# Kernel tuning notes

Measured on AMD Instinct MI355X. Metric: run time of the kernel, lower is better.

Reference implementation:

```python
import jax, jax.numpy as jnp
import numpy as np

B, S, D_IN, D_OUT, H = 8, 512, 1024, 1024, 8
D_ATT = D_OUT // H
NEG_INF = -1e30


def setup_inputs() -> dict:
    key = jax.random.key(0)
    k1, k2, k3, k4 = jax.random.split(key, 4)
    stdv = 1.0 / np.sqrt(D_OUT)
    return {
        "x": jax.random.normal(k1, (B, S, D_IN), dtype=jnp.float32),
        "mask": jnp.ones((B, S), dtype=jnp.float32),
        "adjacency": jax.random.randint(k2, (B, S, S), 0, 2, dtype=jnp.int32),
        "W": jax.random.uniform(k3, (D_IN, D_OUT), dtype=jnp.float32, minval=-stdv, maxval=stdv),
        "att_w": jax.random.normal(k4, (2 * D_ATT,), dtype=jnp.float32) * 0.05,
        "att_b": jnp.zeros((), dtype=jnp.float32),
    }


def reference(x, mask, adjacency, W, att_w, att_b):
    # projection: [B,S,D_IN] @ [D_IN,D_OUT]
    xp = jnp.einsum("bsi,io->bso", x, W)
    # split heads -> [B,H,S,d]
    xh = xp.reshape(B, S, H, D_ATT).transpose(0, 2, 1, 3)
    # LinearMatrixAttention, combination='x,y': sim[i,j] = w1.x_i + w2.x_j + b
    s1 = jnp.einsum("bhsd,d->bhs", xh, att_w[:D_ATT])
    s2 = jnp.einsum("bhsd,d->bhs", xh, att_w[D_ATT:])
    sim = s1[..., :, None] + s2[..., None, :] + att_b  # [B,H,S,S]
    # mask = adjacency AND outer(mask, mask), broadcast over heads
    pair_mask = (adjacency[:, None, :, :] > 0) & (mask[:, None, :, None] > 0) & (mask[:, None, None, :] > 0)
    att = jax.nn.softmax(jnp.where(pair_mask, sim, NEG_INF), axis=-1)
    # weighted sum of values
    out = jnp.einsum("bhij,bhjd->bhid", att, xh)
    out = out.transpose(0, 2, 1, 3).reshape(B, S, D_OUT)
    return out  # activation is identity (None)
```

## Files before the change

kernel.cpp:

```cpp
#include <hip/hip_runtime.h>
#include <hip/hip_bf16.h>

#define B_    8
#define S_    512
#define DIN   1024
#define DOUT  1024
#define H_    8

using bf16x8 = __attribute__((ext_vector_type(8))) short;
using f32x4  = __attribute__((ext_vector_type(4))) float;

__device__ __forceinline__ ushort f2bf(float f) {
  __hip_bfloat16 h = __float2bfloat16(f);
  return *reinterpret_cast<ushort*>(&h);
}
__device__ __forceinline__ float bf2f(ushort u) {
  union { float f; unsigned int i; } v;
  v.i = ((unsigned int)u) << 16;
  return v.f;
}

__device__ __forceinline__ void gld16(const ushort* g, ushort* l) {
  __builtin_amdgcn_global_load_lds(
      (const __attribute__((address_space(1))) unsigned int*)g,
      (__attribute__((address_space(3))) unsigned int*)l, 16, 0, 0);
}

__global__ __launch_bounds__(256) void k_prep(const float* __restrict__ x,
                                              ushort* __restrict__ xbf,
                                              const float* __restrict__ W,
                                              ushort* __restrict__ WT,
                                              const int* __restrict__ adj,
                                              unsigned long long* __restrict__ bm) {
  __shared__ float tile[64][65];
  int blk = blockIdx.x;
  int t = threadIdx.x;
  if (blk < 2048) {
    int i = (blk * 256 + t) * 8;
    const float4* p = reinterpret_cast<const float4*>(x + i);
    float4 a = p[0], b = p[1];
    ushort r[8];
    r[0] = f2bf(a.x); r[1] = f2bf(a.y); r[2] = f2bf(a.z); r[3] = f2bf(a.w);
    r[4] = f2bf(b.x); r[5] = f2bf(b.y); r[6] = f2bf(b.z); r[7] = f2bf(b.w);
    *reinterpret_cast<uint4*>(xbf + i) = *reinterpret_cast<uint4*>(r);
  } else if (blk < 2304) {
    int q = blk - 2048;
    int r0 = (q >> 4) * 64, c0 = (q & 15) * 64;
    int lr = t >> 4, lc = (t & 15) * 4;
#pragma unroll
    for (int i = 0; i < 4; ++i) {
      int row = lr + i * 16;
      float4 v = *reinterpret_cast<const float4*>(&W[(size_t)(r0 + row) * DOUT + c0 + lc]);
      tile[row][lc] = v.x; tile[row][lc + 1] = v.y;
      tile[row][lc + 2] = v.z; tile[row][lc + 3] = v.w;
    }
    __syncthreads();
    int n = t >> 2, ks = (t & 3) * 16;
    ushort o[16];
#pragma unroll
    for (int i = 0; i < 16; ++i) o[i] = f2bf(tile[ks + i][n]);
    ushort* dst = &WT[(size_t)(c0 + n) * DIN + r0 + ks];
    reinterpret_cast<uint4*>(dst)[0] = reinterpret_cast<uint4*>(o)[0];
    reinterpret_cast<uint4*>(dst)[1] = reinterpret_cast<uint4*>(o)[1];
  } else {
    int w = (blk - 2304) * 4 + (t >> 6);
    int lane = t & 63;
    int v = adj[(size_t)w * 64 + lane];
    unsigned long long m = __ballot(v != 0);
    if (lane == 0) bm[w] = m;
  }
}

__global__ __launch_bounds__(256) void k_proj(const ushort* __restrict__ xbf,
                                              const ushort* __restrict__ WT,
                                              const float* __restrict__ attw,
                                              const float* __restrict__ mask,
                                              ushort* __restrict__ xhT,
                                              ushort* __restrict__ ubf) {
  __shared__ __align__(16) ushort As[2 * 64 * 32];
  __shared__ __align__(16) ushort Bs[2 * 128 * 32];
  __shared__ __align__(16) ushort Tr[64 * 130];
  __shared__ float Pp[64 * 4];
  int m0 = blockIdx.x * 64;
  int h  = blockIdx.y;
  int t = threadIdx.x, lane = t & 63, wave = t >> 6;
  int r4 = t >> 2;
  int cswz = (((t & 3) ^ ((r4 >> 1) & 3)) << 3);

  const ushort* ga = &xbf[(size_t)(m0 + r4) * DIN + cswz];
  const ushort* gb = &WT[(size_t)(h * 128 + r4) * DIN + cswz];
  ushort* laA = As + t * 8;
  ushort* laB = Bs + t * 8;
  int rowa = lane & 15;
  int ksw = (((lane >> 4) ^ ((lane >> 1) & 3)) << 3);
  int rbb = wave * 32 + (lane & 15);

  f32x4 acc[4][2] = {};

  for (int kt = 0; kt < DIN; kt += 64) {
    gld16(ga + kt,                 laA);
    gld16(ga + kt + 32,            laA + 2048);
    gld16(gb + kt,                 laB);
    gld16(gb + kt + 64 * DIN,      laB + 2048);
    gld16(gb + kt + 32,            laB + 4096);
    gld16(gb + kt + 32 + 64 * DIN, laB + 6144);
    asm volatile("s_waitcnt vmcnt(0)" ::: "memory");
    __syncthreads();
    bf16x8 a[4][2], bfr[2][2];
#pragma unroll
    for (int mi = 0; mi < 4; ++mi)
#pragma unroll
      for (int ks = 0; ks < 2; ++ks)
        a[mi][ks] = *reinterpret_cast<const bf16x8*>(&As[ks * 2048 + (rowa + mi * 16) * 32 + ksw]);
#pragma unroll
    for (int ni = 0; ni < 2; ++ni)
#pragma unroll
      for (int ks = 0; ks < 2; ++ks)
        bfr[ni][ks] = *reinterpret_cast<const bf16x8*>(&Bs[ks * 4096 + (rbb + ni * 16) * 32 + ksw]);
#pragma unroll
    for (int mi = 0; mi < 4; ++mi)
#pragma unroll
      for (int ni = 0; ni < 2; ++ni)
#pragma unroll
        for (int ks = 0; ks < 2; ++ks)
          acc[mi][ni] = __builtin_amdgcn_mfma_f32_16x16x32_bf16(a[mi][ks], bfr[ni][ks], acc[mi][ni], 0, 0, 0);
    __syncthreads();
  }

  int colb = wave * 32 + (lane & 15);
  int rl = (lane >> 4) * 4;
#pragma unroll
  for (int mi = 0; mi < 4; ++mi)
#pragma unroll
    for (int ni = 0; ni < 2; ++ni) {
      int cc = colb + ni * 16;
#pragma unroll
      for (int j = 0; j < 4; ++j)
        Tr[(mi * 16 + rl + j) * 130 + cc] = f2bf(acc[mi][ni][j]);
    }
  __syncthreads();

  int b = m0 >> 9, s0 = m0 & 511;
  {
    int row = t >> 2, seg = (t & 3) * 32;
    float p = 0.f;
#pragma unroll 8
    for (int d = 0; d < 32; ++d)
      p += bf2f(Tr[row * 130 + seg + d]) * attw[128 + seg + d];
    Pp[row * 4 + (t & 3)] = p;
  }
  {
    int d = t >> 1, sseg = (t & 1) * 32;
    ushort* dst = &xhT[((size_t)(b * H_ + h) * 128 + d) * S_ + s0 + sseg];
#pragma unroll
    for (int g = 0; g < 4; ++g) {
      ushort o[8];
#pragma unroll
      for (int i = 0; i < 8; ++i) o[i] = Tr[(sseg + g * 8 + i) * 130 + d];
      reinterpret_cast<uint4*>(dst)[g] = *reinterpret_cast<uint4*>(o);
    }
  }
  __syncthreads();
  if (t < 64) {
    float s2 = Pp[t * 4] + Pp[t * 4 + 1] + Pp[t * 4 + 2] + Pp[t * 4 + 3];
    float mk = mask[b * S_ + s0 + t];
    float u = (mk > 0.f) ? __expf(s2) : 0.f;
    ubf[(b * H_ + h) * S_ + s0 + t] = f2bf(u);
  }
}

__global__ __launch_bounds__(256) void k_attn(const unsigned long long* __restrict__ bm,
                                              const ushort* __restrict__ xhT,
                                              const ushort* __restrict__ ubf,
                                              float* __restrict__ out) {
  __shared__ __align__(16) ushort As[2 * 64 * 32];
  __shared__ __align__(16) ushort Bs[2 * 128 * 32];
  __shared__ __align__(16) ushort us[512];
  __shared__ float Dred[64 * 4];
  __shared__ float Dsum[64];
  int i0 = blockIdx.x * 64;
  int h  = blockIdx.y;
  int b  = blockIdx.z;
  int t = threadIdx.x, lane = t & 63, wave = t >> 6;

  if (t < 64)
    reinterpret_cast<uint4*>(us)[t] =
        reinterpret_cast<const uint4*>(&ubf[(b * H_ + h) * S_])[t];

  int r4 = t >> 2;
  int cswz = (((t & 3) ^ ((r4 >> 1) & 3)) << 3);
  const ushort* gv = &xhT[((size_t)(b * H_ + h) * 128 + r4) * S_ + cswz];
  ushort* laB = Bs + t * 8;

  int arow = t >> 2, cseg = (t & 3) * 16;
  const unsigned long long* bmrow = &bm[(size_t)(b * S_ + i0 + arow) * 8];
  int s_w = (arow >> 1) & 3;
  int cb = (cseg & 31) >> 3;
  ushort* awbase = As + ((cseg >= 32) ? 2048 : 0) + arow * 32;
  ushort* aw0 = awbase + ((cb ^ s_w) << 3);
  ushort* aw1 = awbase + (((cb + 1) ^ s_w) << 3);

  float dacc = 0.f;
  f32x4 acc[4][2] = {};
  int rowa = lane & 15;
  int ksw = (((lane >> 4) ^ ((lane >> 1) & 3)) << 3);
  int rbb = wave * 32 + (lane & 15);

  __syncthreads();

  for (int kt = 0; kt < S_; kt += 64) {
    gld16(gv + kt,                laB);
    gld16(gv + kt + 64 * S_,      laB + 2048);
    gld16(gv + kt + 32,           laB + 4096);
    gld16(gv + kt + 32 + 64 * S_, laB + 6144);
    unsigned long long w = bmrow[kt >> 6];
    unsigned int bits = (unsigned int)(w >> cseg) & 0xffffu;
    ushort uu[16];
    *reinterpret_cast<uint4*>(uu)     = *reinterpret_cast<const uint4*>(&us[kt + cseg]);
    *reinterpret_cast<uint4*>(uu + 8) = *reinterpret_cast<const uint4*>(&us[kt + cseg + 8]);
    ushort av[16];
#pragma unroll
    for (int q = 0; q < 16; ++q) {
      bool nz = (bits >> q) & 1;
      av[q] = nz ? uu[q] : (ushort)0;
      dacc += nz ? bf2f(uu[q]) : 0.f;
    }
    *reinterpret_cast<uint4*>(aw0) = reinterpret_cast<uint4*>(av)[0];
    *reinterpret_cast<uint4*>(aw1) = reinterpret_cast<uint4*>(av)[1];
    asm volatile("s_waitcnt vmcnt(0)" ::: "memory");
    __syncthreads();
    bf16x8 a[4][2], bfr[2][2];
#pragma unroll
    for (int mi = 0; mi < 4; ++mi)
#pragma unroll
      for (int ks = 0; ks < 2; ++ks)
        a[mi][ks] = *reinterpret_cast<const bf16x8*>(&As[ks * 2048 + (rowa + mi * 16) * 32 + ksw]);
#pragma unroll
    for (int ni = 0; ni < 2; ++ni)
#pragma unroll
      for (int ks = 0; ks < 2; ++ks)
        bfr[ni][ks] = *reinterpret_cast<const bf16x8*>(&Bs[ks * 4096 + (rbb + ni * 16) * 32 + ksw]);
#pragma unroll
    for (int mi = 0; mi < 4; ++mi)
#pragma unroll
      for (int ni = 0; ni < 2; ++ni)
#pragma unroll
        for (int ks = 0; ks < 2; ++ks)
          acc[mi][ni] = __builtin_amdgcn_mfma_f32_16x16x32_bf16(a[mi][ks], bfr[ni][ks], acc[mi][ni], 0, 0, 0);
    __syncthreads();
  }

  Dred[arow * 4 + (t & 3)] = dacc;
  __syncthreads();
  if (t < 64)
    Dsum[t] = Dred[t * 4] + Dred[t * 4 + 1] + Dred[t * 4 + 2] + Dred[t * 4 + 3];
  __syncthreads();

  int colb = wave * 32 + (lane & 15);
  int rl = (lane >> 4) * 4;
#pragma unroll
  for (int mi = 0; mi < 4; ++mi)
#pragma unroll
    for (int ni = 0; ni < 2; ++ni) {
      int cc = colb + ni * 16;
#pragma unroll
      for (int j = 0; j < 4; ++j) {
        int rr = mi * 16 + rl + j;
        float Di = fmaxf(Dsum[rr], 1e-30f);
        out[((size_t)(b * S_ + i0 + rr)) * DOUT + h * 128 + cc] = acc[mi][ni][j] / Di;
      }
    }
}

extern "C" void kernel_launch(void* const* d_in, const int* in_sizes, int n_in,
                              void* d_out, int out_size, void* d_ws, size_t ws_size,
                              hipStream_t stream) {
  const float* x    = (const float*)d_in[0];
  const float* mask = (const float*)d_in[1];
  const int*   adj  = (const int*)d_in[2];
  const float* W    = (const float*)d_in[3];
  const float* attw = (const float*)d_in[4];
  float* out = (float*)d_out;

  char* ws = (char*)d_ws;
  ushort* xbf = (ushort*)ws;
  ushort* WT  = (ushort*)(ws + 8388608);
  ushort* xhT = (ushort*)(ws + 10485760);
  ushort* ubf = (ushort*)(ws + 18874368);
  unsigned long long* bm = (unsigned long long*)(ws + 18939904);

  k_prep<<<dim3(10496), dim3(256), 0, stream>>>(x, xbf, W, WT, adj, bm);
  k_proj<<<dim3(64, 8), dim3(256), 0, stream>>>(xbf, WT, attw, mask, xhT, ubf);
  k_attn<<<dim3(8, 8, 8), dim3(256), 0, stream>>>(bm, xhT, ubf, out);
}
```

Baseline: 119.8 us.

## Double-buffer LDS tiles in projection and attention GEMM loops

Both GEMM kernels now keep two LDS stages. The global-to-LDS loads (and, in attention, the masked A-tile build) for the next K tile are issued before the MFMA work on the current tile. This removes one barrier per iteration and lets memory latency overlap with compute. The cost is more LDS per block (about 48KB), which may lower occupancy, and in the projection kernel the transpose buffer now aliases the A and B tiles.

Result: slower. 122.5 us (+2.3%).

```diff
diff --git a/kernel.cpp b/kernel.cpp
--- a/kernel.cpp
+++ b/kernel.cpp
@@ -77,10 +77,12 @@
                                               const float* __restrict__ mask,
                                               ushort* __restrict__ xhT,
                                               ushort* __restrict__ ubf) {
-  __shared__ __align__(16) ushort As[2 * 64 * 32];
-  __shared__ __align__(16) ushort Bs[2 * 128 * 32];
-  __shared__ __align__(16) ushort Tr[64 * 130];
-  __shared__ float Pp[64 * 4];
+  __shared__ __align__(16) ushort SM[24576];
+  __shared__ float Pp[256];
+  ushort* As = SM;
+  ushort* Bs = SM + 8192;
+  ushort* Tr = SM;
+
   int m0 = blockIdx.x * 64;
   int h  = blockIdx.y;
   int t = threadIdx.x, lane = t & 63, wave = t >> 6;
@@ -89,42 +91,55 @@
 
   const ushort* ga = &xbf[(size_t)(m0 + r4) * DIN + cswz];
   const ushort* gb = &WT[(size_t)(h * 128 + r4) * DIN + cswz];
-  ushort* laA = As + t * 8;
-  ushort* laB = Bs + t * 8;
   int rowa = lane & 15;
   int ksw = (((lane >> 4) ^ ((lane >> 1) & 3)) << 3);
   int rbb = wave * 32 + (lane & 15);
 
   f32x4 acc[4][2] = {};
 
-  for (int kt = 0; kt < DIN; kt += 64) {
-    gld16(ga + kt,                 laA);
-    gld16(ga + kt + 32,            laA + 2048);
-    gld16(gb + kt,                 laB);
-    gld16(gb + kt + 64 * DIN,      laB + 2048);
-    gld16(gb + kt + 32,            laB + 4096);
-    gld16(gb + kt + 32 + 64 * DIN, laB + 6144);
+  auto STAGE = [&](int p, int kt) {
+    ushort* la = As + p * 4096 + t * 8;
+    ushort* lb = Bs + p * 8192 + t * 8;
+    gld16(ga + kt,                 la);
+    gld16(ga + kt + 32,            la + 2048);
+    gld16(gb + kt,                 lb);
+    gld16(gb + kt + 64 * DIN,      lb + 2048);
+    gld16(gb + kt + 32,            lb + 4096);
+    gld16(gb + kt + 32 + 64 * DIN, lb + 6144);
+  };
+  auto COMPUTE = [&](int p) {
+    const ushort* Ab = As + p * 4096;
+    const ushort* Bb = Bs + p * 8192;
+    bf16x8 a[4][2], bfr[2][2];
+#pragma unroll
+    for (int mi = 0; mi < 4; ++mi)
+#pragma unroll
+      for (int ks = 0; ks < 2; ++ks)
+        a[mi][ks] = *reinterpret_cast<const bf16x8*>(&Ab[ks * 2048 + (rowa + mi * 16) * 32 + ksw]);
+#pragma unroll
+    for (int ni = 0; ni < 2; ++ni)
+#pragma unroll
+      for (int ks = 0; ks < 2; ++ks)
+        bfr[ni][ks] = *reinterpret_cast<const bf16x8*>(&Bb[ks * 4096 + (rbb + ni * 16) * 32 + ksw]);
+#pragma unroll
+    for (int mi = 0; mi < 4; ++mi)
+#pragma unroll
+      for (int ni = 0; ni < 2; ++ni)
+#pragma unroll
+        for (int ks = 0; ks < 2; ++ks)
+          acc[mi][ni] = __builtin_amdgcn_mfma_f32_16x16x32_bf16(a[mi][ks], bfr[ni][ks], acc[mi][ni], 0, 0, 0);
+  };
+
+  STAGE(0, 0);
+  asm volatile("s_waitcnt vmcnt(0)" ::: "memory");
+  __syncthreads();
+  int cur = 0;
+  for (int it = 0; it < 16; ++it) {
+    if (it < 15) STAGE(cur ^ 1, (it + 1) * 64);
+    COMPUTE(cur);
     asm volatile("s_waitcnt vmcnt(0)" ::: "memory");
     __syncthreads();
-    bf16x8 a[4][2], bfr[2][2];
-#pragma unroll
-    for (int mi = 0; mi < 4; ++mi)
-#pragma unroll
-      for (int ks = 0; ks < 2; ++ks)
-        a[mi][ks] = *reinterpret_cast<const bf16x8*>(&As[ks * 2048 + (rowa + mi * 16) * 32 + ksw]);
-#pragma unroll
-    for (int ni = 0; ni < 2; ++ni)
-#pragma unroll
-      for (int ks = 0; ks < 2; ++ks)
-        bfr[ni][ks] = *reinterpret_cast<const bf16x8*>(&Bs[ks * 4096 + (rbb + ni * 16) * 32 + ksw]);
-#pragma unroll
-    for (int mi = 0; mi < 4; ++mi)
-#pragma unroll
-      for (int ni = 0; ni < 2; ++ni)
-#pragma unroll
-        for (int ks = 0; ks < 2; ++ks)
-          acc[mi][ni] = __builtin_amdgcn_mfma_f32_16x16x32_bf16(a[mi][ks], bfr[ni][ks], acc[mi][ni], 0, 0, 0);
-    __syncthreads();
+    cur ^= 1;
   }
 
   int colb = wave * 32 + (lane & 15);
@@ -173,11 +188,13 @@
                                               const ushort* __restrict__ xhT,
                                               const ushort* __restrict__ ubf,
                                               float* __restrict__ out) {
-  __shared__ __align__(16) ushort As[2 * 64 * 32];
-  __shared__ __align__(16) ushort Bs[2 * 128 * 32];
+  __shared__ __align__(16) ushort SM[24576];
   __shared__ __align__(16) ushort us[512];
-  __shared__ float Dred[64 * 4];
+  __shared__ float Dred[256];
   __shared__ float Dsum[64];
+  ushort* As = SM;
+  ushort* Bs = SM + 8192;
+
   int i0 = blockIdx.x * 64;
   int h  = blockIdx.y;
   int b  = blockIdx.z;
@@ -190,15 +207,14 @@
   int r4 = t >> 2;
   int cswz = (((t & 3) ^ ((r4 >> 1) & 3)) << 3);
   const ushort* gv = &xhT[((size_t)(b * H_ + h) * 128 + r4) * S_ + cswz];
-  ushort* laB = Bs + t * 8;
 
   int arow = t >> 2, cseg = (t & 3) * 16;
   const unsigned long long* bmrow = &bm[(size_t)(b * S_ + i0 + arow) * 8];
   int s_w = (arow >> 1) & 3;
   int cb = (cseg & 31) >> 3;
-  ushort* awbase = As + ((cseg >= 32) ? 2048 : 0) + arow * 32;
-  ushort* aw0 = awbase + ((cb ^ s_w) << 3);
-  ushort* aw1 = awbase + (((cb + 1) ^ s_w) << 3);
+  int awoff = ((cseg >= 32) ? 2048 : 0) + arow * 32;
+  int aw0o = awoff + (((cb) ^ s_w) << 3);
+  int aw1o = awoff + (((cb + 1) ^ s_w) << 3);
 
   float dacc = 0.f;
   f32x4 acc[4][2] = {};
@@ -206,13 +222,14 @@
   int ksw = (((lane >> 4) ^ ((lane >> 1) & 3)) << 3);
   int rbb = wave * 32 + (lane & 15);
 
-  __syncthreads();
-
-  for (int kt = 0; kt < S_; kt += 64) {
-    gld16(gv + kt,                laB);
-    gld16(gv + kt + 64 * S_,      laB + 2048);
-    gld16(gv + kt + 32,           laB + 4096);
-    gld16(gv + kt + 32 + 64 * S_, laB + 6144);
+  auto STAGEV = [&](int p, int kt) {
+    ushort* lb = Bs + p * 8192 + t * 8;
+    gld16(gv + kt,                lb);
+    gld16(gv + kt + 64 * S_,      lb + 2048);
+    gld16(gv + kt + 32,           lb + 4096);
+    gld16(gv + kt + 32 + 64 * S_, lb + 6144);
+  };
+  auto BUILDA = [&](int p, int kt) {
     unsigned long long w = bmrow[kt >> 6];
     unsigned int bits = (unsigned int)(w >> cseg) & 0xffffu;
     ushort uu[16];
@@ -225,29 +242,48 @@
       av[q] = nz ? uu[q] : (ushort)0;
       dacc += nz ? bf2f(uu[q]) : 0.f;
     }
-    *reinterpret_cast<uint4*>(aw0) = reinterpret_cast<uint4*>(av)[0];
-    *reinterpret_cast<uint4*>(aw1) = reinterpret_cast<uint4*>(av)[1];
+    ushort* ab = As + p * 4096;
+    *reinterpret_cast<uint4*>(ab + aw0o) = reinterpret_cast<uint4*>(av)[0];
+    *reinterpret_cast<uint4*>(ab + aw1o) = reinterpret_cast<uint4*>(av)[1];
+  };
+  auto COMPUTE = [&](int p) {
+    const ushort* Ab = As + p * 4096;
+    const ushort* Bb = Bs + p * 8192;
+    bf16x8 a[4][2], bfr[2][2];
+#pragma unroll
+    for (int mi = 0; mi < 4; ++mi)
+#pragma unroll
+      for (int ks = 0; ks < 2; ++ks)
+        a[mi][ks] = *reinterpret_cast<const bf16x8*>(&Ab[ks * 2048 + (rowa + mi * 16) * 32 + ksw]);
+#pragma unroll
+    for (int ni = 0; ni < 2; ++ni)
+#pragma unroll
+      for (int ks = 0; ks < 2; ++ks)
+        bfr[ni][ks] = *reinterpret_cast<const bf16x8*>(&Bb[ks * 4096 + (rbb + ni * 16) * 32 + ksw]);
+#pragma unroll
+    for (int mi = 0; mi < 4; ++mi)
+#pragma unroll
+      for (int ni = 0; ni < 2; ++ni)
+#pragma unroll
+        for (int ks = 0; ks < 2; ++ks)
+          acc[mi][ni] = __builtin_amdgcn_mfma_f32_16x16x32_bf16(a[mi][ks], bfr[ni][ks], acc[mi][ni], 0, 0, 0);
+  };
+
+  __syncthreads();
+  STAGEV(0, 0);
+  BUILDA(0, 0);
+  asm volatile("s_waitcnt vmcnt(0)" ::: "memory");
+  __syncthreads();
+  int cur = 0;
+  for (int it = 0; it < 8; ++it) {
+    if (it < 7) {
+      STAGEV(cur ^ 1, (it + 1) * 64);
+      BUILDA(cur ^ 1, (it + 1) * 64);
+    }
+    COMPUTE(cur);
     asm volatile("s_waitcnt vmcnt(0)" ::: "memory");
     __syncthreads();
-    bf16x8 a[4][2], bfr[2][2];
-#pragma unroll
-    for (int mi = 0; mi < 4; ++mi)
-#pragma unroll
-      for (int ks = 0; ks < 2; ++ks)
-        a[mi][ks] = *reinterpret_cast<const bf16x8*>(&As[ks * 2048 + (rowa + mi * 16) * 32 + ksw]);
-#pragma unroll
-    for (int ni = 0; ni < 2; ++ni)
-#pragma unroll
-      for (int ks = 0; ks < 2; ++ks)
-        bfr[ni][ks] = *reinterpret_cast<const bf16x8*>(&Bs[ks * 4096 + (rbb + ni * 16) * 32 + ksw]);
-#pragma unroll
-    for (int mi = 0; mi < 4; ++mi)
-#pragma unroll
-      for (int ni = 0; ni < 2; ++ni)
-#pragma unroll
-        for (int ks = 0; ks < 2; ++ks)
-          acc[mi][ni] = __builtin_amdgcn_mfma_f32_16x16x32_bf16(a[mi][ks], bfr[ni][ks], acc[mi][ni], 0, 0, 0);
-    __syncthreads();
+    cur ^= 1;
   }
 
   Dred[arow * 4 + (t & 3)] = dacc;
```

## Merge prep, projection and attention kernels into one cooperative kernel with grid syncs

Applied to the files above, without the earlier changes.

Replaces the three separate kernel launches with a single cooperative persistent kernel of 512 blocks. The prep, projection and attention phases are separated by grid-wide barriers, and shared memory is aliased across phases. This removes launch gaps and inter-kernel drain, but the prep phase now runs on 512 blocks looping instead of ~10k blocks. It also adds grid.sync overhead and requires all 512 blocks to be co-resident.

Measured after the change: 351.4 us. 2.93x slower.

```diff
diff --git a/kernel.cpp b/kernel.cpp
--- a/kernel.cpp
+++ b/kernel.cpp
@@ -1,5 +1,8 @@
 #include <hip/hip_runtime.h>
 #include <hip/hip_bf16.h>
+#include <hip/hip_cooperative_groups.h>
+
+namespace cg = cooperative_groups;
 
 #define B_    8
 #define S_    512
@@ -26,250 +29,259 @@
       (__attribute__((address_space(3))) unsigned int*)l, 16, 0, 0);
 }
 
-__global__ __launch_bounds__(256) void k_prep(const float* __restrict__ x,
+__global__ __launch_bounds__(256) void k_mega(const float* __restrict__ x,
                                               ushort* __restrict__ xbf,
                                               const float* __restrict__ W,
                                               ushort* __restrict__ WT,
                                               const int* __restrict__ adj,
-                                              unsigned long long* __restrict__ bm) {
-  __shared__ float tile[64][65];
-  int blk = blockIdx.x;
-  int t = threadIdx.x;
-  if (blk < 2048) {
-    int i = (blk * 256 + t) * 8;
-    const float4* p = reinterpret_cast<const float4*>(x + i);
-    float4 a = p[0], b = p[1];
-    ushort r[8];
-    r[0] = f2bf(a.x); r[1] = f2bf(a.y); r[2] = f2bf(a.z); r[3] = f2bf(a.w);
-    r[4] = f2bf(b.x); r[5] = f2bf(b.y); r[6] = f2bf(b.z); r[7] = f2bf(b.w);
-    *reinterpret_cast<uint4*>(xbf + i) = *reinterpret_cast<uint4*>(r);
-  } else if (blk < 2304) {
-    int q = blk - 2048;
-    int r0 = (q >> 4) * 64, c0 = (q & 15) * 64;
-    int lr = t >> 4, lc = (t & 15) * 4;
-#pragma unroll
-    for (int i = 0; i < 4; ++i) {
-      int row = lr + i * 16;
-      float4 v = *reinterpret_cast<const float4*>(&W[(size_t)(r0 + row) * DOUT + c0 + lc]);
-      tile[row][lc] = v.x; tile[row][lc + 1] = v.y;
-      tile[row][lc + 2] = v.z; tile[row][lc + 3] = v.w;
-    }
-    __syncthreads();
-    int n = t >> 2, ks = (t & 3) * 16;
-    ushort o[16];
-#pragma unroll
-    for (int i = 0; i < 16; ++i) o[i] = f2bf(tile[ks + i][n]);
-    ushort* dst = &WT[(size_t)(c0 + n) * DIN + r0 + ks];
-    reinterpret_cast<uint4*>(dst)[0] = reinterpret_cast<uint4*>(o)[0];
-    reinterpret_cast<uint4*>(dst)[1] = reinterpret_cast<uint4*>(o)[1];
-  } else {
-    int w = (blk - 2304) * 4 + (t >> 6);
-    int lane = t & 63;
-    int v = adj[(size_t)w * 64 + lane];
-    unsigned long long m = __ballot(v != 0);
-    if (lane == 0) bm[w] = m;
-  }
-}
-
-__global__ __launch_bounds__(256) void k_proj(const ushort* __restrict__ xbf,
-                                              const ushort* __restrict__ WT,
+                                              unsigned long long* __restrict__ bm,
                                               const float* __restrict__ attw,
                                               const float* __restrict__ mask,
                                               ushort* __restrict__ xhT,
-                                              ushort* __restrict__ ubf) {
-  __shared__ __align__(16) ushort As[2 * 64 * 32];
-  __shared__ __align__(16) ushort Bs[2 * 128 * 32];
-  __shared__ __align__(16) ushort Tr[64 * 130];
-  __shared__ float Pp[64 * 4];
-  int m0 = blockIdx.x * 64;
-  int h  = blockIdx.y;
+                                              ushort* __restrict__ ubf,
+                                              float* __restrict__ out) {
+  __shared__ __align__(16) char SMEM[27648];
+  cg::grid_group grid = cg::this_grid();
+  int blk = blockIdx.x;
   int t = threadIdx.x, lane = t & 63, wave = t >> 6;
-  int r4 = t >> 2;
-  int cswz = (((t & 3) ^ ((r4 >> 1) & 3)) << 3);
-
-  const ushort* ga = &xbf[(size_t)(m0 + r4) * DIN + cswz];
-  const ushort* gb = &WT[(size_t)(h * 128 + r4) * DIN + cswz];
-  ushort* laA = As + t * 8;
-  ushort* laB = Bs + t * 8;
-  int rowa = lane & 15;
-  int ksw = (((lane >> 4) ^ ((lane >> 1) & 3)) << 3);
-  int rbb = wave * 32 + (lane & 15);
-
-  f32x4 acc[4][2] = {};
-
-  for (int kt = 0; kt < DIN; kt += 64) {
-    gld16(ga + kt,                 laA);
-    gld16(ga + kt + 32,            laA + 2048);
-    gld16(gb + kt,                 laB);
-    gld16(gb + kt + 64 * DIN,      laB + 2048);
-    gld16(gb + kt + 32,            laB + 4096);
-    gld16(gb + kt + 32 + 64 * DIN, laB + 6144);
-    asm volatile("s_waitcnt vmcnt(0)" ::: "memory");
-    __syncthreads();
-    bf16x8 a[4][2], bfr[2][2];
+
+  {
+#pragma unroll
+    for (int pass = 0; pass < 4; ++pass) {
+      int i = (pass * 131072 + blk * 256 + t) * 8;
+      const float4* p = reinterpret_cast<const float4*>(x + i);
+      float4 a = p[0], b = p[1];
+      ushort r[8];
+      r[0] = f2bf(a.x); r[1] = f2bf(a.y); r[2] = f2bf(a.z); r[3] = f2bf(a.w);
+      r[4] = f2bf(b.x); r[5] = f2bf(b.y); r[6] = f2bf(b.z); r[7] = f2bf(b.w);
+      *reinterpret_cast<uint4*>(xbf + i) = *reinterpret_cast<uint4*>(r);
+    }
+    if (blk < 256) {
+      float (*tile)[65] = reinterpret_cast<float(*)[65]>(SMEM);
+      int r0 = (blk >> 4) * 64, c0 = (blk & 15) * 64;
+      int lr = t >> 4, lc = (t & 15) * 4;
+#pragma unroll
+      for (int i = 0; i < 4; ++i) {
+        int row = lr + i * 16;
+        float4 v = *reinterpret_cast<const float4*>(&W[(size_t)(r0 + row) * DOUT + c0 + lc]);
+        tile[row][lc] = v.x; tile[row][lc + 1] = v.y;
+        tile[row][lc + 2] = v.z; tile[row][lc + 3] = v.w;
+      }
+      __syncthreads();
+      int n = t >> 2, ks = (t & 3) * 16;
+      ushort o[16];
+#pragma unroll
+      for (int i = 0; i < 16; ++i) o[i] = f2bf(tile[ks + i][n]);
+      ushort* dst = &WT[(size_t)(c0 + n) * DIN + r0 + ks];
+      reinterpret_cast<uint4*>(dst)[0] = reinterpret_cast<uint4*>(o)[0];
+      reinterpret_cast<uint4*>(dst)[1] = reinterpret_cast<uint4*>(o)[1];
+    }
+    int grp = wave;
+#pragma unroll
+    for (int it = 0; it < 16; ++it) {
+      int w = it * 2048 + blk * 4 + grp;
+      int v = adj[(size_t)w * 64 + lane];
+      unsigned long long m = __ballot(v != 0);
+      if (lane == 0) bm[w] = m;
+    }
+  }
+  __threadfence();
+  grid.sync();
+
+  {
+    ushort* As = reinterpret_cast<ushort*>(SMEM);
+    ushort* Bs = reinterpret_cast<ushort*>(SMEM + 8192);
+    ushort* Tr = reinterpret_cast<ushort*>(SMEM);
+    float*  Pp = reinterpret_cast<float*>(SMEM + 24576);
+
+    int m0 = (blk >> 3) * 64;
+    int h  = blk & 7;
+    int r4 = t >> 2;
+    int cswz = (((t & 3) ^ ((r4 >> 1) & 3)) << 3);
+
+    const ushort* ga = &xbf[(size_t)(m0 + r4) * DIN + cswz];
+    const ushort* gb = &WT[(size_t)(h * 128 + r4) * DIN + cswz];
+    ushort* laA = As + t * 8;
+    ushort* laB = Bs + t * 8;
+    int rowa = lane & 15;
+    int ksw = (((lane >> 4) ^ ((lane >> 1) & 3)) << 3);
+    int rbb = wave * 32 + (lane & 15);
+
+    f32x4 acc[4][2] = {};
+
+    for (int kt = 0; kt < DIN; kt += 64) {
+      gld16(ga + kt,                 laA);
+      gld16(ga + kt + 32,            laA + 2048);
+      gld16(gb + kt,                 laB);
+      gld16(gb + kt + 64 * DIN,      laB + 2048);
+      gld16(gb + kt + 32,            laB + 4096);
+      gld16(gb + kt + 32 + 64 * DIN, laB + 6144);
+      asm volatile("s_waitcnt vmcnt(0)" ::: "memory");
+      __syncthreads();
+      bf16x8 a[4][2], bfr[2][2];
+#pragma unroll
+      for (int mi = 0; mi < 4; ++mi)
+#pragma unroll
+        for (int ks = 0; ks < 2; ++ks)
+          a[mi][ks] = *reinterpret_cast<const bf16x8*>(&As[ks * 2048 + (rowa + mi * 16) * 32 + ksw]);
+#pragma unroll
+      for (int ni = 0; ni < 2; ++ni)
+#pragma unroll
+        for (int ks = 0; ks < 2; ++ks)
+          bfr[ni][ks] = *reinterpret_cast<const bf16x8*>(&Bs[ks * 4096 + (rbb + ni * 16) * 32 + ksw]);
+#pragma unroll
+      for (int mi = 0; mi < 4; ++mi)
+#pragma unroll
+        for (int ni = 0; ni < 2; ++ni)
+#pragma unroll
+          for (int ks = 0; ks < 2; ++ks)
+            acc[mi][ni] = __builtin_amdgcn_mfma_f32_16x16x32_bf16(a[mi][ks], bfr[ni][ks], acc[mi][ni], 0, 0, 0);
+      __syncthreads();
+    }
+
+    int colb = wave * 32 + (lane & 15);
+    int rl = (lane >> 4) * 4;
 #pragma unroll
     for (int mi = 0; mi < 4; ++mi)
 #pragma unroll
-      for (int ks = 0; ks < 2; ++ks)
-        a[mi][ks] = *reinterpret_cast<const bf16x8*>(&As[ks * 2048 + (rowa + mi * 16) * 32 + ksw]);
-#pragma unroll
-    for (int ni = 0; ni < 2; ++ni)
-#pragma unroll
-      for (int ks = 0; ks < 2; ++ks)
-        bfr[ni][ks] = *reinterpret_cast<const bf16x8*>(&Bs[ks * 4096 + (rbb + ni * 16) * 32 + ksw]);
+      for (int ni = 0; ni < 2; ++ni) {
+        int cc = colb + ni * 16;
+#pragma unroll
+        for (int j = 0; j < 4; ++j)
+          Tr[(mi * 16 + rl + j) * 130 + cc] = f2bf(acc[mi][ni][j]);
+      }
+    __syncthreads();
+
+    int b = m0 >> 9, s0 = m0 & 511;
+    {
+      int row = t >> 2, seg = (t & 3) * 32;
+      float p = 0.f;
+#pragma unroll 8
+      for (int d = 0; d < 32; ++d)
+        p += bf2f(Tr[row * 130 + seg + d]) * attw[128 + seg + d];
+      Pp[row * 4 + (t & 3)] = p;
+    }
+    {
+      int d = t >> 1, sseg = (t & 1) * 32;
+      ushort* dst = &xhT[((size_t)(b * H_ + h) * 128 + d) * S_ + s0 + sseg];
+#pragma unroll
+      for (int g = 0; g < 4; ++g) {
+        ushort o[8];
+#pragma unroll
+        for (int i = 0; i < 8; ++i) o[i] = Tr[(sseg + g * 8 + i) * 130 + d];
+        reinterpret_cast<uint4*>(dst)[g] = *reinterpret_cast<uint4*>(o);
+      }
+    }
+    __syncthreads();
+    if (t < 64) {
+      float s2 = Pp[t * 4] + Pp[t * 4 + 1] + Pp[t * 4 + 2] + Pp[t * 4 + 3];
+      float mk = mask[b * S_ + s0 + t];
+      float u = (mk > 0.f) ? __expf(s2) : 0.f;
+      ubf[(b * H_ + h) * S_ + s0 + t] = f2bf(u);
+    }
+  }
+  __threadfence();
+  grid.sync();
+
+  {
+    ushort* As = reinterpret_cast<ushort*>(SMEM);
+    ushort* Bs = reinterpret_cast<ushort*>(SMEM + 8192);
+    ushort* us = reinterpret_cast<ushort*>(SMEM + 24576);
+    float* Dred = reinterpret_cast<float*>(SMEM + 25600);
+    float* Dsum = reinterpret_cast<float*>(SMEM + 26624);
+
+    int b  = blk >> 6;
+    int h  = (blk >> 3) & 7;
+    int i0 = (blk & 7) * 64;
+
+    if (t < 64)
+      reinterpret_cast<uint4*>(us)[t] =
+          reinterpret_cast<const uint4*>(&ubf[(b * H_ + h) * S_])[t];
+
+    int r4 = t >> 2;
+    int cswz = (((t & 3) ^ ((r4 >> 1) & 3)) << 3);
+    const ushort* gv = &xhT[((size_t)(b * H_ + h) * 128 + r4) * S_ + cswz];
+    ushort* laB = Bs + t * 8;
+
+    int arow = t >> 2, cseg = (t & 3) * 16;
+    const unsigned long long* bmrow = &bm[(size_t)(b * S_ + i0 + arow) * 8];
+    int s_w = (arow >> 1) & 3;
+    int cb = (cseg & 31) >> 3;
+    ushort* awbase = As + ((cseg >= 32) ? 2048 : 0) + arow * 32;
+    ushort* aw0 = awbase + (((cb) ^ s_w) << 3);
+    ushort* aw1 = awbase + (((cb + 1) ^ s_w) << 3);
+
+    float dacc = 0.f;
+    f32x4 acc[4][2] = {};
+    int rowa = lane & 15;
+    int ksw = (((lane >> 4) ^ ((lane >> 1) & 3)) << 3);
+    int rbb = wave * 32 + (lane & 15);
+
+    __syncthreads();
+
+    for (int kt = 0; kt < S_; kt += 64) {
+      gld16(gv + kt,                laB);
+      gld16(gv + kt + 64 * S_,      laB + 2048);
+      gld16(gv + kt + 32,           laB + 4096);
+      gld16(gv + kt + 32 + 64 * S_, laB + 6144);
+      unsigned long long w = bmrow[kt >> 6];
+      unsigned int bits = (unsigned int)(w >> cseg) & 0xffffu;
+      ushort uu[16];
+      *reinterpret_cast<uint4*>(uu)     = *reinterpret_cast<const uint4*>(&us[kt + cseg]);
+      *reinterpret_cast<uint4*>(uu + 8) = *reinterpret_cast<const uint4*>(&us[kt + cseg + 8]);
+      ushort av[16];
+#pragma unroll
+      for (int q = 0; q < 16; ++q) {
+        bool nz = (bits >> q) & 1;
+        av[q] = nz ? uu[q] : (ushort)0;
+        dacc += nz ? bf2f(uu[q]) : 0.f;
+      }
+      *reinterpret_cast<uint4*>(aw0) = reinterpret_cast<uint4*>(av)[0];
+      *reinterpret_cast<uint4*>(aw1) = reinterpret_cast<uint4*>(av)[1];
+      asm volatile("s_waitcnt vmcnt(0)" ::: "memory");
+      __syncthreads();
+      bf16x8 a[4][2], bfr[2][2];
+#pragma unroll
+      for (int mi = 0; mi < 4; ++mi)
+#pragma unroll
+        for (int ks = 0; ks < 2; ++ks)
+          a[mi][ks] = *reinterpret_cast<const bf16x8*>(&As[ks * 2048 + (rowa + mi * 16) * 32 + ksw]);
+#pragma unroll
+      for (int ni = 0; ni < 2; ++ni)
+#pragma unroll
+        for (int ks = 0; ks < 2; ++ks)
+          bfr[ni][ks] = *reinterpret_cast<const bf16x8*>(&Bs[ks * 4096 + (rbb + ni * 16) * 32 + ksw]);
+#pragma unroll
+      for (int mi = 0; mi < 4; ++mi)
+#pragma unroll
+        for (int ni = 0; ni < 2; ++ni)
+#pragma unroll
+          for (int ks = 0; ks < 2; ++ks)
+            acc[mi][ni] = __builtin_amdgcn_mfma_f32_16x16x32_bf16(a[mi][ks], bfr[ni][ks], acc[mi][ni], 0, 0, 0);
+      __syncthreads();
+    }
+
+    Dred[arow * 4 + (t & 3)] = dacc;
+    __syncthreads();
+    if (t < 64)
+      Dsum[t] = Dred[t * 4] + Dred[t * 4 + 1] + Dred[t * 4 + 2] + Dred[t * 4 + 3];
+    __syncthreads();
+
+    int colb = wave * 32 + (lane & 15);
+    int rl = (lane >> 4) * 4;
 #pragma unroll
     for (int mi = 0; mi < 4; ++mi)
 #pragma unroll
-      for (int ni = 0; ni < 2; ++ni)
-#pragma unroll
-        for (int ks = 0; ks < 2; ++ks)
-          acc[mi][ni] = __builtin_amdgcn_mfma_f32_16x16x32_bf16(a[mi][ks], bfr[ni][ks], acc[mi][ni], 0, 0, 0);
-    __syncthreads();
+      for (int ni = 0; ni < 2; ++ni) {
+        int cc = colb + ni * 16;
+#pragma unroll
+        for (int j = 0; j < 4; ++j) {
+          int rr = mi * 16 + rl + j;
+          float Di = fmaxf(Dsum[rr], 1e-30f);
+          out[((size_t)(b * S_ + i0 + rr)) * DOUT + h * 128 + cc] = acc[mi][ni][j] / Di;
+        }
+      }
   }
-
-  int colb = wave * 32 + (lane & 15);
-  int rl = (lane >> 4) * 4;
-#pragma unroll
-  for (int mi = 0; mi < 4; ++mi)
-#pragma unroll
-    for (int ni = 0; ni < 2; ++ni) {
-      int cc = colb + ni * 16;
-#pragma unroll
-      for (int j = 0; j < 4; ++j)
-        Tr[(mi * 16 + rl + j) * 130 + cc] = f2bf(acc[mi][ni][j]);
-    }
-  __syncthreads();
-
-  int b = m0 >> 9, s0 = m0 & 511;
-  {
-    int row = t >> 2, seg = (t & 3) * 32;
-    float p = 0.f;
-#pragma unroll 8
-    for (int d = 0; d < 32; ++d)
-      p += bf2f(Tr[row * 130 + seg + d]) * attw[128 + seg + d];
-    Pp[row * 4 + (t & 3)] = p;
-  }
-  {
-    int d = t >> 1, sseg = (t & 1) * 32;
-    ushort* dst = &xhT[((size_t)(b * H_ + h) * 128 + d) * S_ + s0 + sseg];
-#pragma unroll
-    for (int g = 0; g < 4; ++g) {
-      ushort o[8];
-#pragma unroll
-      for (int i = 0; i < 8; ++i) o[i] = Tr[(sseg + g * 8 + i) * 130 + d];
-      reinterpret_cast<uint4*>(dst)[g] = *reinterpret_cast<uint4*>(o);
-    }
-  }
-  __syncthreads();
-  if (t < 64) {
-    float s2 = Pp[t * 4] + Pp[t * 4 + 1] + Pp[t * 4 + 2] + Pp[t * 4 + 3];
-    float mk = mask[b * S_ + s0 + t];
-    float u = (mk > 0.f) ? __expf(s2) : 0.f;
-    ubf[(b * H_ + h) * S_ + s0 + t] = f2bf(u);
-  }
-}
-
-__global__ __launch_bounds__(256) void k_attn(const unsigned long long* __restrict__ bm,
-                                              const ushort* __restrict__ xhT,
-                                              const ushort* __restrict__ ubf,
-                                              float* __restrict__ out) {
-  __shared__ __align__(16) ushort As[2 * 64 * 32];
-  __shared__ __align__(16) ushort Bs[2 * 128 * 32];
-  __shared__ __align__(16) ushort us[512];
-  __shared__ float Dred[64 * 4];
-  __shared__ float Dsum[64];
-  int i0 = blockIdx.x * 64;
-  int h  = blockIdx.y;
-  int b  = blockIdx.z;
-  int t = threadIdx.x, lane = t & 63, wave = t >> 6;
-
-  if (t < 64)
-    reinterpret_cast<uint4*>(us)[t] =
-        reinterpret_cast<const uint4*>(&ubf[(b * H_ + h) * S_])[t];
-
-  int r4 = t >> 2;
-  int cswz = (((t & 3) ^ ((r4 >> 1) & 3)) << 3);
-  const ushort* gv = &xhT[((size_t)(b * H_ + h) * 128 + r4) * S_ + cswz];
-  ushort* laB = Bs + t * 8;
-
-  int arow = t >> 2, cseg = (t & 3) * 16;
-  const unsigned long long* bmrow = &bm[(size_t)(b * S_ + i0 + arow) * 8];
-  int s_w = (arow >> 1) & 3;
-  int cb = (cseg & 31) >> 3;
-  ushort* awbase = As + ((cseg >= 32) ? 2048 : 0) + arow * 32;
-  ushort* aw0 = awbase + ((cb ^ s_w) << 3);
-  ushort* aw1 = awbase + (((cb + 1) ^ s_w) << 3);
-
-  float dacc = 0.f;
-  f32x4 acc[4][2] = {};
-  int rowa = lane & 15;
-  int ksw = (((lane >> 4) ^ ((lane >> 1) & 3)) << 3);
-  int rbb = wave * 32 + (lane & 15);
-
-  __syncthreads();
-
-  for (int kt = 0; kt < S_; kt += 64) {
-    gld16(gv + kt,                laB);
-    gld16(gv + kt + 64 * S_,      laB + 2048);
-    gld16(gv + kt + 32,           laB + 4096);
-    gld16(gv + kt + 32 + 64 * S_, laB + 6144);
-    unsigned long long w = bmrow[kt >> 6];
-    unsigned int bits = (unsigned int)(w >> cseg) & 0xffffu;
-    ushort uu[16];
-    *reinterpret_cast<uint4*>(uu)     = *reinterpret_cast<const uint4*>(&us[kt + cseg]);
-    *reinterpret_cast<uint4*>(uu + 8) = *reinterpret_cast<const uint4*>(&us[kt + cseg + 8]);
-    ushort av[16];
-#pragma unroll
-    for (int q = 0; q < 16; ++q) {
-      bool nz = (bits >> q) & 1;
-      av[q] = nz ? uu[q] : (ushort)0;
-      dacc += nz ? bf2f(uu[q]) : 0.f;
-    }
-    *reinterpret_cast<uint4*>(aw0) = reinterpret_cast<uint4*>(av)[0];
-    *reinterpret_cast<uint4*>(aw1) = reinterpret_cast<uint4*>(av)[1];
-    asm volatile("s_waitcnt vmcnt(0)" ::: "memory");
-    __syncthreads();
-    bf16x8 a[4][2], bfr[2][2];
-#pragma unroll
-    for (int mi = 0; mi < 4; ++mi)
-#pragma unroll
-      for (int ks = 0; ks < 2; ++ks)
-        a[mi][ks] = *reinterpret_cast<const bf16x8*>(&As[ks * 2048 + (rowa + mi * 16) * 32 + ksw]);
-#pragma unroll
-    for (int ni = 0; ni < 2; ++ni)
-#pragma unroll
-      for (int ks = 0; ks < 2; ++ks)
-        bfr[ni][ks] = *reinterpret_cast<const bf16x8*>(&Bs[ks * 4096 + (rbb + ni * 16) * 32 + ksw]);
-#pragma unroll
-    for (int mi = 0; mi < 4; ++mi)
-#pragma unroll
-      for (int ni = 0; ni < 2; ++ni)
-#pragma unroll
-        for (int ks = 0; ks < 2; ++ks)
-          acc[mi][ni] = __builtin_amdgcn_mfma_f32_16x16x32_bf16(a[mi][ks], bfr[ni][ks], acc[mi][ni], 0, 0, 0);
-    __syncthreads();
-  }
-
-  Dred[arow * 4 + (t & 3)] = dacc;
-  __syncthreads();
-  if (t < 64)
-    Dsum[t] = Dred[t * 4] + Dred[t * 4 + 1] + Dred[t * 4 + 2] + Dred[t * 4 + 3];
-  __syncthreads();
-
-  int colb = wave * 32 + (lane & 15);
-  int rl = (lane >> 4) * 4;
-#pragma unroll
-  for (int mi = 0; mi < 4; ++mi)
-#pragma unroll
-    for (int ni = 0; ni < 2; ++ni) {
-      int cc = colb + ni * 16;
-#pragma unroll
-      for (int j = 0; j < 4; ++j) {
-        int rr = mi * 16 + rl + j;
-        float Di = fmaxf(Dsum[rr], 1e-30f);
-        out[((size_t)(b * S_ + i0 + rr)) * DOUT + h * 128 + cc] = acc[mi][ni][j] / Di;
-      }
-    }
 }
 
 extern "C" void kernel_launch(void* const* d_in, const int* in_sizes, int n_in,
@@ -289,7 +301,9 @@
   ushort* ubf = (ushort*)(ws + 18874368);
   unsigned long long* bm = (unsigned long long*)(ws + 18939904);
 
-  k_prep<<<dim3(10496), dim3(256), 0, stream>>>(x, xbf, W, WT, adj, bm);
-  k_proj<<<dim3(64, 8), dim3(256), 0, stream>>>(xbf, WT, attw, mask, xhT, ubf);
-  k_attn<<<dim3(8, 8, 8), dim3(256), 0, stream>>>(bm, xhT, ubf, out);
-}
+  void* args[] = {(void*)&x, (void*)&xbf, (void*)&W, (void*)&WT, (void*)&adj,
+                  (void*)&bm, (void*)&attw, (void*)&mask, (void*)&xhT,
+                  (void*)&ubf, (void*)&out};
+  hipLaunchCooperativeKernel((const void*)k_mega, dim3(512), dim3(256),
+                             args, 0, stream);
+}
```

## Fuse x fp32-to-bf16 conversion into projection GEMM and reorder attention grid

Applied to the files above, without the earlier changes.

Drops the separate pass that converts x to bf16 in the prep kernel. The projection kernel now loads fp32 x directly, converts it in registers and stores it to LDS, which removes one 16MB read, an 8MB write and the 8MB bf16 re-read. The cost is that every head block (8 of them) reads the fp32 x tile, so GEMM A-side traffic doubles and the A loads become synchronous register loads instead of async direct-to-LDS loads. The attention grid is also reordered to put head and batch on the fastest dimensions, which changes how blocks are scheduled and how they hit the cache.

New measurement: 121.5 us. No clear change (+1.4%).

```diff
diff --git a/kernel.cpp b/kernel.cpp
--- a/kernel.cpp
+++ b/kernel.cpp
@@ -26,26 +26,15 @@
       (__attribute__((address_space(3))) unsigned int*)l, 16, 0, 0);
 }
 
-__global__ __launch_bounds__(256) void k_prep(const float* __restrict__ x,
-                                              ushort* __restrict__ xbf,
-                                              const float* __restrict__ W,
+__global__ __launch_bounds__(256) void k_prep(const float* __restrict__ W,
                                               ushort* __restrict__ WT,
                                               const int* __restrict__ adj,
                                               unsigned long long* __restrict__ bm) {
   __shared__ float tile[64][65];
   int blk = blockIdx.x;
   int t = threadIdx.x;
-  if (blk < 2048) {
-    int i = (blk * 256 + t) * 8;
-    const float4* p = reinterpret_cast<const float4*>(x + i);
-    float4 a = p[0], b = p[1];
-    ushort r[8];
-    r[0] = f2bf(a.x); r[1] = f2bf(a.y); r[2] = f2bf(a.z); r[3] = f2bf(a.w);
-    r[4] = f2bf(b.x); r[5] = f2bf(b.y); r[6] = f2bf(b.z); r[7] = f2bf(b.w);
-    *reinterpret_cast<uint4*>(xbf + i) = *reinterpret_cast<uint4*>(r);
-  } else if (blk < 2304) {
-    int q = blk - 2048;
-    int r0 = (q >> 4) * 64, c0 = (q & 15) * 64;
+  if (blk < 256) {
+    int r0 = (blk >> 4) * 64, c0 = (blk & 15) * 64;
     int lr = t >> 4, lc = (t & 15) * 4;
 #pragma unroll
     for (int i = 0; i < 4; ++i) {
@@ -63,7 +52,7 @@
     reinterpret_cast<uint4*>(dst)[0] = reinterpret_cast<uint4*>(o)[0];
     reinterpret_cast<uint4*>(dst)[1] = reinterpret_cast<uint4*>(o)[1];
   } else {
-    int w = (blk - 2304) * 4 + (t >> 6);
+    int w = (blk - 256) * 4 + (t >> 6);
     int lane = t & 63;
     int v = adj[(size_t)w * 64 + lane];
     unsigned long long m = __ballot(v != 0);
@@ -71,7 +60,7 @@
   }
 }
 
-__global__ __launch_bounds__(256) void k_proj(const ushort* __restrict__ xbf,
+__global__ __launch_bounds__(256) void k_proj(const float* __restrict__ x,
                                               const ushort* __restrict__ WT,
                                               const float* __restrict__ attw,
                                               const float* __restrict__ mask,
@@ -87,9 +76,8 @@
   int r4 = t >> 2;
   int cswz = (((t & 3) ^ ((r4 >> 1) & 3)) << 3);
 
-  const ushort* ga = &xbf[(size_t)(m0 + r4) * DIN + cswz];
+  const float*  gx = &x[(size_t)(m0 + r4) * DIN + cswz];
   const ushort* gb = &WT[(size_t)(h * 128 + r4) * DIN + cswz];
-  ushort* laA = As + t * 8;
   ushort* laB = Bs + t * 8;
   int rowa = lane & 15;
   int ksw = (((lane >> 4) ^ ((lane >> 1) & 3)) << 3);
@@ -98,12 +86,21 @@
   f32x4 acc[4][2] = {};
 
   for (int kt = 0; kt < DIN; kt += 64) {
-    gld16(ga + kt,                 laA);
-    gld16(ga + kt + 32,            laA + 2048);
+    float4 a0 = *reinterpret_cast<const float4*>(gx + kt);
+    float4 a1 = *reinterpret_cast<const float4*>(gx + kt + 4);
+    float4 b0 = *reinterpret_cast<const float4*>(gx + kt + 32);
+    float4 b1 = *reinterpret_cast<const float4*>(gx + kt + 36);
     gld16(gb + kt,                 laB);
     gld16(gb + kt + 64 * DIN,      laB + 2048);
     gld16(gb + kt + 32,            laB + 4096);
     gld16(gb + kt + 32 + 64 * DIN, laB + 6144);
+    ushort r0[8], r1[8];
+    r0[0] = f2bf(a0.x); r0[1] = f2bf(a0.y); r0[2] = f2bf(a0.z); r0[3] = f2bf(a0.w);
+    r0[4] = f2bf(a1.x); r0[5] = f2bf(a1.y); r0[6] = f2bf(a1.z); r0[7] = f2bf(a1.w);
+    r1[0] = f2bf(b0.x); r1[1] = f2bf(b0.y); r1[2] = f2bf(b0.z); r1[3] = f2bf(b0.w);
+    r1[4] = f2bf(b1.x); r1[5] = f2bf(b1.y); r1[6] = f2bf(b1.z); r1[7] = f2bf(b1.w);
+    *reinterpret_cast<uint4*>(&As[t * 8])        = *reinterpret_cast<uint4*>(r0);
+    *reinterpret_cast<uint4*>(&As[t * 8 + 2048]) = *reinterpret_cast<uint4*>(r1);
     asm volatile("s_waitcnt vmcnt(0)" ::: "memory");
     __syncthreads();
     bf16x8 a[4][2], bfr[2][2];
@@ -178,9 +175,9 @@
   __shared__ __align__(16) ushort us[512];
   __shared__ float Dred[64 * 4];
   __shared__ float Dsum[64];
-  int i0 = blockIdx.x * 64;
-  int h  = blockIdx.y;
-  int b  = blockIdx.z;
+  int h  = blockIdx.x;
+  int b  = blockIdx.y;
+  int i0 = blockIdx.z * 64;
   int t = threadIdx.x, lane = t & 63, wave = t >> 6;
 
   if (t < 64)
@@ -197,7 +194,7 @@
   int s_w = (arow >> 1) & 3;
   int cb = (cseg & 31) >> 3;
   ushort* awbase = As + ((cseg >= 32) ? 2048 : 0) + arow * 32;
-  ushort* aw0 = awbase + ((cb ^ s_w) << 3);
+  ushort* aw0 = awbase + (((cb) ^ s_w) << 3);
   ushort* aw1 = awbase + (((cb + 1) ^ s_w) << 3);
 
   float dacc = 0.f;
@@ -283,13 +280,12 @@
   float* out = (float*)d_out;
 
   char* ws = (char*)d_ws;
-  ushort* xbf = (ushort*)ws;
-  ushort* WT  = (ushort*)(ws + 8388608);
-  ushort* xhT = (ushort*)(ws + 10485760);
-  ushort* ubf = (ushort*)(ws + 18874368);
-  unsigned long long* bm = (unsigned long long*)(ws + 18939904);
-
-  k_prep<<<dim3(10496), dim3(256), 0, stream>>>(x, xbf, W, WT, adj, bm);
-  k_proj<<<dim3(64, 8), dim3(256), 0, stream>>>(xbf, WT, attw, mask, xhT, ubf);
+  ushort* WT  = (ushort*)ws;
+  ushort* xhT = (ushort*)(ws + 2097152);
+  ushort* ubf = (ushort*)(ws + 10485760);
+  unsigned long long* bm = (unsigned long long*)(ws + 10551296);
+
+  k_prep<<<dim3(8448), dim3(256), 0, stream>>>(W, WT, adj, bm);
+  k_proj<<<dim3(64, 8), dim3(256), 0, stream>>>(x, WT, attw, mask, xhT, ubf);
   k_attn<<<dim3(8, 8, 8), dim3(256), 0, stream>>>(bm, xhT, ubf, out);
 }
```
